# Kernel optimization log

Hardware: AMD Instinct MI355X
Metric: run time of the kernel (lower is better)

The kernel has to match this reference:

```python
import jax, jax.numpy as jnp
import numpy as np

H = 16
EMB = 1024
DH = 64  # att_dim


def setup_inputs() -> dict:
    key = jax.random.key(0)
    k1, k2, k3 = jax.random.split(key, 3)
    B, T = 4, 2048
    x = jax.random.normal(k1, (B, T, EMB), dtype=jnp.float32)
    # torch nn.Linear weight layout: [out_features, in_features]
    w_qkv = jax.random.normal(k2, (3 * H * DH, EMB), dtype=jnp.float32) * (1.0 / np.sqrt(EMB))
    wo = jax.random.normal(k3, (EMB, H * DH), dtype=jnp.float32) * (1.0 / np.sqrt(H * DH))
    return {"x": x, "w_qkv": w_qkv, "wo": wo}


def reference(x, w_qkv, wo):
    B, T, C = x.shape
    qkv = jnp.einsum('btc,oc->bto', x, w_qkv)  # [B,T,3*H*DH]
    q, k, v = jnp.split(qkv, 3, axis=-1)
    # [B,H,T,DH]
    q = q.reshape(B, T, H, DH).transpose(0, 2, 1, 3)
    k = k.reshape(B, T, H, DH).transpose(0, 2, 1, 3)
    v = v.reshape(B, T, H, DH).transpose(0, 2, 1, 3)
    scale = 1.0 / np.sqrt(DH).astype(np.float32)
    scores = jnp.einsum('bhqd,bhkd->bhqk', q, k) * scale
    causal = jnp.tril(jnp.ones((T, T), dtype=bool))
    scores = jnp.where(causal, scores, jnp.finfo(scores.dtype).min)
    attn = jax.nn.softmax(scores, axis=-1)
    y = jnp.einsum('bhqk,bhkd->bhqd', attn, v)  # [B,H,T,DH]
    y = y.transpose(0, 2, 1, 3).reshape(B, T, H * DH)
    return jnp.einsum('bti,oi->bto', y, wo)
```

## Files before the change

### kernel.cpp

```cpp
#include <hip/hip_runtime.h>
#include <hip/hip_bf16.h>
#include <stdint.h>


typedef __attribute__((ext_vector_type(8))) short short8;
typedef __attribute__((ext_vector_type(4))) float floatx4;

extern "C" __device__ float __ocml_native_exp2_f32(float);

__device__ __forceinline__ ushort f2bf(float f) {
  uint32_t u = __float_as_uint(f);
  u += 0x7fff + ((u >> 16) & 1);
  return (ushort)(u >> 16);
}

#if __has_builtin(__builtin_amdgcn_cvt_pk_bf16_f32)
typedef __attribute__((ext_vector_type(2))) __bf16 bf16x2;
__device__ __forceinline__ uint32_t pack_bf16(float a, float b) {
  union { bf16x2 v; uint32_t u; } cv;
  cv.v = __builtin_amdgcn_cvt_pk_bf16_f32(a, b);
  return cv.u;
}
#else
__device__ __forceinline__ uint32_t pack_bf16(float a, float b) {
  uint32_t ua = __float_as_uint(a) + 0x8000u;
  uint32_t ub = __float_as_uint(b) + 0x8000u;
  return __builtin_amdgcn_perm(ub, ua, 0x07060302u);
}
#endif

__device__ __forceinline__ void gload16(const ushort* g, ushort* l) {
  __builtin_amdgcn_global_load_lds(
      (const __attribute__((address_space(1))) void*)g,
      (__attribute__((address_space(3))) void*)l, 16, 0, 0);
}

__global__ __launch_bounds__(256) void cvt3_kernel(const float* __restrict__ x,
                                                   const float* __restrict__ wq,
                                                   const float* __restrict__ wo,
                                                   ushort* __restrict__ xo,
                                                   ushort* __restrict__ wqo,
                                                   ushort* __restrict__ woo) {
  int i = blockIdx.x * 256 + threadIdx.x;
  const float* in; ushort* out; int idx;
  if (i < 2097152)      { in = x;  out = xo;  idx = i; }
  else if (i < 2883584) { in = wq; out = wqo; idx = i - 2097152; }
  else                  { in = wo; out = woo; idx = i - 2883584; }
  float4 v = ((const float4*)in)[idx];
  ushort4 o;
  o.x = f2bf(v.x); o.y = f2bf(v.y); o.z = f2bf(v.z); o.w = f2bf(v.w);
  ((ushort4*)out)[idx] = o;
}

template<int MODE>
__global__ __launch_bounds__(256) void gemm_bt(const ushort* __restrict__ A,
                                               const ushort* __restrict__ Bw,
                                               float* __restrict__ Cf,
                                               ushort* __restrict__ qb,
                                               ushort* __restrict__ kb,
                                               ushort* __restrict__ vt) {
  constexpr int CS = 136;
  constexpr int SMEM_N = (MODE == 0) ? 128 * CS : 128 * 64 * 2;
  __shared__ ushort smem[SMEM_N];
  ushort* As = smem;
  ushort* Bs = smem + 128 * 64;
  int tid = threadIdx.x;
  int lane = tid & 63, wave = tid >> 6;
  int lrow = lane & 15, quad = lane >> 4;
  int wr = (wave >> 1) * 64, wc = (wave & 1) * 64;
  int m0 = blockIdx.x * 128, n0 = blockIdx.y * 128;

  const floatx4 zero4 = {0.f, 0.f, 0.f, 0.f};
  floatx4 acc[4][4];
#pragma unroll
  for (int i = 0; i < 4; i++)
#pragma unroll
    for (int j = 0; j < 4; j++) acc[i][j] = zero4;

  int rsub = tid >> 3;
  int colb = (((tid & 7) ^ (rsub & 7)) * 8);
  const ushort* Ag = A + (size_t)(m0 + rsub) * 1024 + colb;
  const ushort* Bg = Bw + (size_t)(n0 + rsub) * 1024 + colb;
  int fo = (quad ^ (lrow & 7)) * 8;

  for (int kk = 0; kk < 1024; kk += 64) {
    __syncthreads();
#pragma unroll
    for (int i = 0; i < 4; i++) {
      gload16(Ag + kk + (size_t)i * 32 * 1024, &As[(8 * wave + 32 * i) * 64]);
      gload16(Bg + kk + (size_t)i * 32 * 1024, &Bs[(8 * wave + 32 * i) * 64]);
    }
    __syncthreads();
#pragma unroll
    for (int ks = 0; ks < 2; ks++) {
      short8 a[4], b[4];
#pragma unroll
      for (int i = 0; i < 4; i++)
        a[i] = *(const short8*)(&As[(wr + i * 16 + lrow) * 64 + (fo ^ (32 * ks))]);
#pragma unroll
      for (int j = 0; j < 4; j++)
        b[j] = *(const short8*)(&Bs[(wc + j * 16 + lrow) * 64 + (fo ^ (32 * ks))]);
#pragma unroll
      for (int i = 0; i < 4; i++)
#pragma unroll
        for (int j = 0; j < 4; j++)
          acc[i][j] = __builtin_amdgcn_mfma_f32_16x16x32_bf16(a[i], b[j], acc[i][j], 0, 0, 0);
    }
  }

  if (MODE == 1) {
#pragma unroll
    for (int i = 0; i < 4; i++)
#pragma unroll
      for (int j = 0; j < 4; j++)
#pragma unroll
        for (int r = 0; r < 4; r++) {
          int m = m0 + wr + i * 16 + quad * 4 + r;
          int n = n0 + wc + j * 16 + lrow;
          Cf[(size_t)m * 1024 + n] = acc[i][j][r];
        }
    return;
  }

  int sec = n0 >> 10;
  __syncthreads();

  if (sec < 2) {
    float qs = (sec == 0) ? 0.18033688f : 1.0f;
#pragma unroll
    for (int i = 0; i < 4; i++)
#pragma unroll
      for (int j = 0; j < 4; j++)
#pragma unroll
        for (int r = 0; r < 4; r++)
          smem[(wr + i * 16 + quad * 4 + r) * CS + wc + j * 16 + lrow] =
              f2bf(acc[i][j][r] * qs);
    __syncthreads();
    ushort* dst = (sec == 0) ? qb : kb;
    int mrow = tid >> 3, kcol = tid & 7;
#pragma unroll
    for (int mi = 0; mi < 4; mi++)
#pragma unroll
      for (int hh = 0; hh < 2; hh++) {
        int mloc = mi * 32 + mrow;
        uint4 val = *(const uint4*)(&smem[mloc * CS + hh * 64 + kcol * 8]);
        int m = m0 + mloc, b = m >> 11, t = m & 2047;
        int h = ((n0 + hh * 64) & 1023) >> 6;
        *(uint4*)(dst + ((size_t)(b * 16 + h) * 2048 + t) * 64 + kcol * 8) = val;
      }
  } else {
#pragma unroll
    for (int i = 0; i < 4; i++)
#pragma unroll
      for (int j = 0; j < 4; j++) {
        uint2 w;
        w.x = pack_bf16(acc[i][j][0], acc[i][j][1]);
        w.y = pack_bf16(acc[i][j][2], acc[i][j][3]);
        *(uint2*)(&smem[(wc + j * 16 + lrow) * CS + wr + i * 16 + quad * 4]) = w;
      }
    __syncthreads();
    int b = m0 >> 11, t0 = m0 & 2047;
    int drow = tid >> 4, kcol = tid & 15;
#pragma unroll
    for (int di = 0; di < 8; di++) {
      int nloc = di * 16 + drow;
      uint4 val = *(const uint4*)(&smem[nloc * CS + kcol * 8]);
      int n = n0 + nloc;
      int h = (n & 1023) >> 6, d = n & 63;
      *(uint4*)(vt + ((size_t)(b * 16 + h) * 64 + d) * 2048 + t0 + kcol * 8) = val;
    }
  }
}

__global__ __launch_bounds__(256) void attn_kernel(const ushort* __restrict__ qg,
                                                   const ushort* __restrict__ kg,
                                                   const ushort* __restrict__ vg,
                                                   ushort* __restrict__ y) {
  __shared__ ushort Ks[64 * 64];
  __shared__ ushort Vs[64 * 64];
  __shared__ ushort QPs[4608];
  int tid = threadIdx.x;
  int lane = tid & 63, wave = tid >> 6;
  int lrow = lane & 15, quad = lane >> 4;
  int gx = blockIdx.x, gy = blockIdx.y;
  int qt = 31 - (gy >> 3);
  int bh = (gy & 7) * 8 + gx;
  const ushort* qp = qg + (size_t)bh * 2048 * 64;
  const ushort* kp = kg + (size_t)bh * 2048 * 64;
  const ushort* vp = vg + (size_t)bh * 64 * 2048;
  int b = bh >> 4, h = bh & 15;
  int l8 = lane >> 3;
  int gswz = ((lane & 7) ^ (l8 & 7)) * 8;
  int fo = (quad ^ (lrow & 7)) * 8;
  ushort* Pw = &QPs[wave * 16 * 72];

#pragma unroll
  for (int i = 0; i < 2; i++) {
    int v = tid + 256 * i;
    int row = v >> 3, c = v & 7;
    *(uint4*)(&QPs[row * 64 + ((c ^ (row & 7)) * 8)]) =
        *(const uint4*)(qp + (size_t)(qt * 64 + row) * 64 + c * 8);
  }
  __syncthreads();
  short8 a_q0 = *(const short8*)(&QPs[(wave * 16 + lrow) * 64 + fo]);
  short8 a_q1 = *(const short8*)(&QPs[(wave * 16 + lrow) * 64 + (fo ^ 32)]);

  const floatx4 zero4 = {0.f, 0.f, 0.f, 0.f};
  short8 ones;
#pragma unroll
  for (int i = 0; i < 8; i++) ones[i] = (short)0x3F80;
  floatx4 l_acc = zero4;
  floatx4 o_acc[4];
#pragma unroll
  for (int j = 0; j < 4; j++) o_acc[j] = zero4;

  for (int kv = 0; kv <= qt; kv++) {
    __syncthreads();
#pragma unroll
    for (int i = 0; i < 2; i++) {
      gload16(kp + (size_t)(kv * 64 + 8 * wave + 32 * i + l8) * 64 + gswz,
              &Ks[(8 * wave + 32 * i) * 64]);
      gload16(vp + (size_t)(8 * wave + 32 * i + l8) * 2048 + kv * 64 + gswz,
              &Vs[(8 * wave + 32 * i) * 64]);
    }
    __syncthreads();

    floatx4 s[4];
#pragma unroll
    for (int ct = 0; ct < 4; ct++) {
      short8 k0 = *(const short8*)(&Ks[(ct * 16 + lrow) * 64 + fo]);
      short8 k1 = *(const short8*)(&Ks[(ct * 16 + lrow) * 64 + (fo ^ 32)]);
      floatx4 z = zero4;
      z = __builtin_amdgcn_mfma_f32_16x16x32_bf16(k0, a_q0, z, 0, 0, 0);
      z = __builtin_amdgcn_mfma_f32_16x16x32_bf16(k1, a_q1, z, 0, 0, 0);
      s[ct] = z;
    }

    if (kv == qt) {
      int qrow = wave * 16 + lrow;
#pragma unroll
      for (int ct = 0; ct < 4; ct++)
#pragma unroll
        for (int r = 0; r < 4; r++)
          if (ct * 16 + quad * 4 + r > qrow) s[ct][r] = -1e30f;
    }

#pragma unroll
    for (int ct = 0; ct < 4; ct++) {
      float p0 = __ocml_native_exp2_f32(s[ct][0]);
      float p1 = __ocml_native_exp2_f32(s[ct][1]);
      float p2 = __ocml_native_exp2_f32(s[ct][2]);
      float p3 = __ocml_native_exp2_f32(s[ct][3]);
      uint2 w;
      w.x = pack_bf16(p0, p1);
      w.y = pack_bf16(p2, p3);
      *(uint2*)(&Pw[lrow * 72 + ct * 16 + quad * 4]) = w;
    }
    asm volatile("" ::: "memory");

    short8 a_p0 = *(const short8*)(&Pw[lrow * 72 + quad * 8]);
    short8 a_p1 = *(const short8*)(&Pw[lrow * 72 + 32 + quad * 8]);
    l_acc = __builtin_amdgcn_mfma_f32_16x16x32_bf16(a_p0, ones, l_acc, 0, 0, 0);
    l_acc = __builtin_amdgcn_mfma_f32_16x16x32_bf16(a_p1, ones, l_acc, 0, 0, 0);
#pragma unroll
    for (int j = 0; j < 4; j++) {
      short8 v0 = *(const short8*)(&Vs[(j * 16 + lrow) * 64 + fo]);
      short8 v1 = *(const short8*)(&Vs[(j * 16 + lrow) * 64 + (fo ^ 32)]);
      o_acc[j] = __builtin_amdgcn_mfma_f32_16x16x32_bf16(a_p0, v0, o_acc[j], 0, 0, 0);
      o_acc[j] = __builtin_amdgcn_mfma_f32_16x16x32_bf16(a_p1, v1, o_acc[j], 0, 0, 0);
    }
  }

  float inv[4];
#pragma unroll
  for (int r = 0; r < 4; r++) inv[r] = 1.0f / l_acc[r];

#pragma unroll
  for (int j = 0; j < 4; j++)
#pragma unroll
    for (int r = 0; r < 4; r++) {
      int t = qt * 64 + wave * 16 + quad * 4 + r;
      y[((size_t)b * 2048 + t) * 1024 + h * 64 + j * 16 + lrow] =
          f2bf(o_acc[j][r] * inv[r]);
    }
}

extern "C" void kernel_launch(void* const* d_in, const int* in_sizes, int n_in,
                              void* d_out, int out_size, void* d_ws, size_t ws_size,
                              hipStream_t stream) {
  const float* x     = (const float*)d_in[0];
  const float* w_qkv = (const float*)d_in[1];
  const float* wo    = (const float*)d_in[2];
  float* out = (float*)d_out;

  ushort* x_bf    = (ushort*)d_ws;
  ushort* wqkv_bf = x_bf + (size_t)8192 * 1024;
  ushort* wo_bf   = wqkv_bf + (size_t)3072 * 1024;
  ushort* qb      = wo_bf + (size_t)1024 * 1024;
  ushort* kb      = qb + (size_t)8388608;
  ushort* vt      = kb + (size_t)8388608;
  ushort* yb      = x_bf;

  cvt3_kernel<<<12288, 256, 0, stream>>>(x, w_qkv, wo, x_bf, wqkv_bf, wo_bf);
  gemm_bt<0><<<dim3(64, 24), 256, 0, stream>>>(x_bf, wqkv_bf, nullptr, qb, kb, vt);
  attn_kernel<<<dim3(8, 256), 256, 0, stream>>>(qb, kb, vt, yb);
  gemm_bt<1><<<dim3(64, 8), 256, 0, stream>>>(yb, wo_bf, out, nullptr, nullptr, nullptr);
}
```

Before: 229.4 us.

## Restructure attention into 128-row Q tiles with paired causal passes and register prefetch

Each attention block now has 512 threads (8 waves) covering 128 query rows, and it handles two query tiles (pr and 15-pr) one after the other so causal work is balanced across blocks. Q is loaded directly from global into registers with no LDS staging. The next K/V tile is prefetched into registers while the current tile is computed, replacing the async LDS loads. The intent is to share each K/V tile across more query rows, balance the causal workload, and hide global load latency. The cost is a larger block with more threads per barrier, and only 512 blocks in the grid.

Result: faster. 219.5 us (-4.3%).

```diff
diff --git a/kernel.cpp b/kernel.cpp
--- a/kernel.cpp
+++ b/kernel.cpp
@@ -172,117 +172,121 @@
   }
 }
 
-__global__ __launch_bounds__(256) void attn_kernel(const ushort* __restrict__ qg,
+__global__ __launch_bounds__(512) void attn_kernel(const ushort* __restrict__ qg,
                                                    const ushort* __restrict__ kg,
                                                    const ushort* __restrict__ vg,
                                                    ushort* __restrict__ y) {
   __shared__ ushort Ks[64 * 64];
   __shared__ ushort Vs[64 * 64];
-  __shared__ ushort QPs[4608];
+  __shared__ ushort Ps[8 * 16 * 72];
   int tid = threadIdx.x;
   int lane = tid & 63, wave = tid >> 6;
   int lrow = lane & 15, quad = lane >> 4;
   int gx = blockIdx.x, gy = blockIdx.y;
-  int qt = 31 - (gy >> 3);
+  int pr = gy >> 3;
   int bh = (gy & 7) * 8 + gx;
   const ushort* qp = qg + (size_t)bh * 2048 * 64;
   const ushort* kp = kg + (size_t)bh * 2048 * 64;
   const ushort* vp = vg + (size_t)bh * 64 * 2048;
   int b = bh >> 4, h = bh & 15;
-  int l8 = lane >> 3;
-  int gswz = ((lane & 7) ^ (l8 & 7)) * 8;
+  int srow = tid >> 3, sc = tid & 7;
+  int sswz = ((sc ^ (srow & 7)) * 8);
   int fo = (quad ^ (lrow & 7)) * 8;
-  ushort* Pw = &QPs[wave * 16 * 72];
-
-#pragma unroll
-  for (int i = 0; i < 2; i++) {
-    int v = tid + 256 * i;
-    int row = v >> 3, c = v & 7;
-    *(uint4*)(&QPs[row * 64 + ((c ^ (row & 7)) * 8)]) =
-        *(const uint4*)(qp + (size_t)(qt * 64 + row) * 64 + c * 8);
-  }
-  __syncthreads();
-  short8 a_q0 = *(const short8*)(&QPs[(wave * 16 + lrow) * 64 + fo]);
-  short8 a_q1 = *(const short8*)(&QPs[(wave * 16 + lrow) * 64 + (fo ^ 32)]);
+  ushort* Pw = &Ps[wave * 16 * 72];
 
   const floatx4 zero4 = {0.f, 0.f, 0.f, 0.f};
   short8 ones;
 #pragma unroll
   for (int i = 0; i < 8; i++) ones[i] = (short)0x3F80;
-  floatx4 l_acc = zero4;
-  floatx4 o_acc[4];
-#pragma unroll
-  for (int j = 0; j < 4; j++) o_acc[j] = zero4;
-
-  for (int kv = 0; kv <= qt; kv++) {
-    __syncthreads();
-#pragma unroll
-    for (int i = 0; i < 2; i++) {
-      gload16(kp + (size_t)(kv * 64 + 8 * wave + 32 * i + l8) * 64 + gswz,
-              &Ks[(8 * wave + 32 * i) * 64]);
-      gload16(vp + (size_t)(8 * wave + 32 * i + l8) * 2048 + kv * 64 + gswz,
-              &Vs[(8 * wave + 32 * i) * 64]);
+
+#pragma unroll 1
+  for (int pass = 0; pass < 2; ++pass) {
+    int qt = pass ? (15 - pr) : pr;
+    int last = 2 * qt + 1;
+
+    const ushort* qrow_p = qp + (size_t)((qt << 7) + wave * 16 + lrow) * 64;
+    short8 a_q0 = *(const short8*)(qrow_p + quad * 8);
+    short8 a_q1 = *(const short8*)(qrow_p + (quad ^ 4) * 8);
+
+    uint4 kreg = *(const uint4*)(kp + (size_t)srow * 64 + sc * 8);
+    uint4 vreg = *(const uint4*)(vp + (size_t)srow * 2048 + sc * 8);
+
+    floatx4 l_acc = zero4;
+    floatx4 o_acc[4];
+#pragma unroll
+    for (int j = 0; j < 4; j++) o_acc[j] = zero4;
+
+#pragma unroll 1
+    for (int kv = 0; kv <= last; kv++) {
+      __syncthreads();
+      *(uint4*)(&Ks[srow * 64 + sswz]) = kreg;
+      *(uint4*)(&Vs[srow * 64 + sswz]) = vreg;
+      if (kv < last) {
+        kreg = *(const uint4*)(kp + (size_t)((kv + 1) * 64 + srow) * 64 + sc * 8);
+        vreg = *(const uint4*)(vp + (size_t)srow * 2048 + (kv + 1) * 64 + sc * 8);
+      }
+      __syncthreads();
+
+      floatx4 s[4];
+#pragma unroll
+      for (int ct = 0; ct < 4; ct++) {
+        short8 k0 = *(const short8*)(&Ks[(ct * 16 + lrow) * 64 + fo]);
+        short8 k1 = *(const short8*)(&Ks[(ct * 16 + lrow) * 64 + (fo ^ 32)]);
+        floatx4 z = zero4;
+        z = __builtin_amdgcn_mfma_f32_16x16x32_bf16(k0, a_q0, z, 0, 0, 0);
+        z = __builtin_amdgcn_mfma_f32_16x16x32_bf16(k1, a_q1, z, 0, 0, 0);
+        s[ct] = z;
+      }
+
+      if (kv >= 2 * qt) {
+        int qabs = (qt << 7) + wave * 16 + lrow;
+        int kbase = (kv << 6) + quad * 4;
+#pragma unroll
+        for (int ct = 0; ct < 4; ct++)
+#pragma unroll
+          for (int r = 0; r < 4; r++)
+            if (kbase + ct * 16 + r > qabs) s[ct][r] = -1e30f;
+      }
+
+#pragma unroll
+      for (int ct = 0; ct < 4; ct++) {
+        float p0 = __ocml_native_exp2_f32(s[ct][0]);
+        float p1 = __ocml_native_exp2_f32(s[ct][1]);
+        float p2 = __ocml_native_exp2_f32(s[ct][2]);
+        float p3 = __ocml_native_exp2_f32(s[ct][3]);
+        uint2 w;
+        w.x = pack_bf16(p0, p1);
+        w.y = pack_bf16(p2, p3);
+        *(uint2*)(&Pw[lrow * 72 + ct * 16 + quad * 4]) = w;
+      }
+      asm volatile("" ::: "memory");
+
+      short8 a_p0 = *(const short8*)(&Pw[lrow * 72 + quad * 8]);
+      short8 a_p1 = *(const short8*)(&Pw[lrow * 72 + 32 + quad * 8]);
+      l_acc = __builtin_amdgcn_mfma_f32_16x16x32_bf16(a_p0, ones, l_acc, 0, 0, 0);
+      l_acc = __builtin_amdgcn_mfma_f32_16x16x32_bf16(a_p1, ones, l_acc, 0, 0, 0);
+#pragma unroll
+      for (int j = 0; j < 4; j++) {
+        short8 v0 = *(const short8*)(&Vs[(j * 16 + lrow) * 64 + fo]);
+        short8 v1 = *(const short8*)(&Vs[(j * 16 + lrow) * 64 + (fo ^ 32)]);
+        o_acc[j] = __builtin_amdgcn_mfma_f32_16x16x32_bf16(a_p0, v0, o_acc[j], 0, 0, 0);
+        o_acc[j] = __builtin_amdgcn_mfma_f32_16x16x32_bf16(a_p1, v1, o_acc[j], 0, 0, 0);
+      }
     }
-    __syncthreads();
-
-    floatx4 s[4];
-#pragma unroll
-    for (int ct = 0; ct < 4; ct++) {
-      short8 k0 = *(const short8*)(&Ks[(ct * 16 + lrow) * 64 + fo]);
-      short8 k1 = *(const short8*)(&Ks[(ct * 16 + lrow) * 64 + (fo ^ 32)]);
-      floatx4 z = zero4;
-      z = __builtin_amdgcn_mfma_f32_16x16x32_bf16(k0, a_q0, z, 0, 0, 0);
-      z = __builtin_amdgcn_mfma_f32_16x16x32_bf16(k1, a_q1, z, 0, 0, 0);
-      s[ct] = z;
-    }
-
-    if (kv == qt) {
-      int qrow = wave * 16 + lrow;
-#pragma unroll
-      for (int ct = 0; ct < 4; ct++)
-#pragma unroll
-        for (int r = 0; r < 4; r++)
-          if (ct * 16 + quad * 4 + r > qrow) s[ct][r] = -1e30f;
-    }
-
-#pragma unroll
-    for (int ct = 0; ct < 4; ct++) {
-      float p0 = __ocml_native_exp2_f32(s[ct][0]);
-      float p1 = __ocml_native_exp2_f32(s[ct][1]);
-      float p2 = __ocml_native_exp2_f32(s[ct][2]);
-      float p3 = __ocml_native_exp2_f32(s[ct][3]);
-      uint2 w;
-      w.x = pack_bf16(p0, p1);
-      w.y = pack_bf16(p2, p3);
-      *(uint2*)(&Pw[lrow * 72 + ct * 16 + quad * 4]) = w;
-    }
-    asm volatile("" ::: "memory");
-
-    short8 a_p0 = *(const short8*)(&Pw[lrow * 72 + quad * 8]);
-    short8 a_p1 = *(const short8*)(&Pw[lrow * 72 + 32 + quad * 8]);
-    l_acc = __builtin_amdgcn_mfma_f32_16x16x32_bf16(a_p0, ones, l_acc, 0, 0, 0);
-    l_acc = __builtin_amdgcn_mfma_f32_16x16x32_bf16(a_p1, ones, l_acc, 0, 0, 0);
-#pragma unroll
-    for (int j = 0; j < 4; j++) {
-      short8 v0 = *(const short8*)(&Vs[(j * 16 + lrow) * 64 + fo]);
-      short8 v1 = *(const short8*)(&Vs[(j * 16 + lrow) * 64 + (fo ^ 32)]);
-      o_acc[j] = __builtin_amdgcn_mfma_f32_16x16x32_bf16(a_p0, v0, o_acc[j], 0, 0, 0);
-      o_acc[j] = __builtin_amdgcn_mfma_f32_16x16x32_bf16(a_p1, v1, o_acc[j], 0, 0, 0);
-    }
+
+    float inv[4];
+#pragma unroll
+    for (int r = 0; r < 4; r++) inv[r] = 1.0f / l_acc[r];
+
+#pragma unroll
+    for (int j = 0; j < 4; j++)
+#pragma unroll
+      for (int r = 0; r < 4; r++) {
+        int t = (qt << 7) + wave * 16 + quad * 4 + r;
+        y[((size_t)b * 2048 + t) * 1024 + h * 64 + j * 16 + lrow] =
+            f2bf(o_acc[j][r] * inv[r]);
+      }
   }
-
-  float inv[4];
-#pragma unroll
-  for (int r = 0; r < 4; r++) inv[r] = 1.0f / l_acc[r];
-
-#pragma unroll
-  for (int j = 0; j < 4; j++)
-#pragma unroll
-    for (int r = 0; r < 4; r++) {
-      int t = qt * 64 + wave * 16 + quad * 4 + r;
-      y[((size_t)b * 2048 + t) * 1024 + h * 64 + j * 16 + lrow] =
-          f2bf(o_acc[j][r] * inv[r]);
-    }
 }
 
 extern "C" void kernel_launch(void* const* d_in, const int* in_sizes, int n_in,
@@ -303,6 +307,6 @@
 
   cvt3_kernel<<<12288, 256, 0, stream>>>(x, w_qkv, wo, x_bf, wqkv_bf, wo_bf);
   gemm_bt<0><<<dim3(64, 24), 256, 0, stream>>>(x_bf, wqkv_bf, nullptr, qb, kb, vt);
-  attn_kernel<<<dim3(8, 256), 256, 0, stream>>>(qb, kb, vt, yb);
+  attn_kernel<<<dim3(8, 64), 512, 0, stream>>>(qb, kb, vt, yb);
   gemm_bt<1><<<dim3(64, 8), 256, 0, stream>>>(yb, wo_bf, out, nullptr, nullptr, nullptr);
 }
```
